# Performance work log

Measured on AMD Instinct MI355X. Metric: run time of the kernel, lower is better.

## Reference

```python
import jax, jax.numpy as jnp
import numpy as np

N, E, G, H, C, DIN, DE = 20000, 320000, 32, 8, 56, 32, 5
HC = H * C  # 448
NEG_SLOPE = 0.2
EPS_BN = 1e-5


def _seg_softmax(scores, seg, num):
    # scores: [E, H], softmax over edges sharing the same target node
    m = jax.ops.segment_max(scores, seg, num_segments=num)
    e = jnp.exp(scores - m[seg])
    s = jax.ops.segment_sum(e, seg, num_segments=num)
    return e / (s[seg] + 1e-16)


def _add_self_loops(src, dst, eattr, n):
    # PyG fill_value='mean': self-loop edge_attr = mean of incoming edge_attr
    deg = jax.ops.segment_sum(jnp.ones((src.shape[0],), eattr.dtype), dst, num_segments=n)
    esum = jax.ops.segment_sum(eattr, dst, num_segments=n)
    loop_attr = esum / jnp.maximum(deg, 1.0)[:, None]
    ar = jnp.arange(n, dtype=src.dtype)
    return (jnp.concatenate([src, ar]), jnp.concatenate([dst, ar]),
            jnp.concatenate([eattr, loop_attr], axis=0))


def _gatv2(x, src, dst, eattr, Wl, Wr, We, att, bias, n):
    xl = (x @ Wl).reshape(n, H, C)  # source transform (messages)
    xr = (x @ Wr).reshape(n, H, C)  # target transform
    ee = (eattr @ We).reshape(-1, H, C)
    s = jax.nn.leaky_relu(xl[src] + xr[dst] + ee, NEG_SLOPE)  # [E, H, C]
    score = jnp.einsum('ehc,hc->eh', s, att)
    alpha = _seg_softmax(score, dst, n)
    out = jax.ops.segment_sum(alpha[..., None] * xl[src], dst, num_segments=n)
    return out.reshape(n, HC) + bias


def _bn(x, gamma, beta):
    m = x.mean(axis=0)
    v = x.var(axis=0)  # biased variance, as torch BatchNorm1d (training)
    return (x - m) * jax.lax.rsqrt(v + EPS_BN) * gamma + beta


def setup_inputs() -> dict:
    key = jax.random.key(0)
    ks = jax.random.split(key, 18)
    sc = lambda k, shape: (jax.random.normal(k, shape, jnp.float32) * 0.05)
    return {
        'x': jax.random.normal(ks[0], (N, DIN), jnp.float32),
        'edge_index': jax.random.randint(ks[1], (2, E), 0, N),
        'edge_attr': jax.random.normal(ks[2], (E, DE), jnp.float32),
        'batch': jnp.sort(jax.random.randint(ks[3], (N,), 0, G)),
        'Wl1': sc(ks[4], (DIN, HC)), 'Wr1': sc(ks[5], (DIN, HC)),
        'We1': sc(ks[6], (DE, HC)), 'att1': sc(ks[7], (H, C)),
        'bias1': jnp.zeros((HC,), jnp.float32),
        'Wl2': sc(ks[8], (HC, HC)), 'Wr2': sc(ks[9], (HC, HC)),
        'We2': sc(ks[10], (DE, HC)), 'att2': sc(ks[11], (H, C)),
        'bias2': jnp.zeros((HC,), jnp.float32),
        'bn_gamma': jnp.ones((HC,), jnp.float32),
        'bn_beta': jnp.zeros((HC,), jnp.float32),
        'Wlin': sc(ks[12], (HC, 18)),
        'blin': jnp.zeros((18,), jnp.float32),
    }


def reference(x, edge_index, edge_attr, batch, Wl1, Wr1, We1, att1, bias1,
              Wl2, Wr2, We2, att2, bias2, bn_gamma, bn_beta, Wlin, blin):
    src, dst = edge_index[0], edge_index[1]
    src2, dst2, ea2 = _add_self_loops(src, dst, edge_attr, N)
    # dropout is identity in eval
    h = _gatv2(x, src2, dst2, ea2, Wl1, Wr1, We1, att1, bias1, N)
    h = jax.nn.elu(h)
    h = _bn(h, bn_gamma, bn_beta)
    h = _gatv2(h, src2, dst2, ea2, Wl2, Wr2, We2, att2, bias2, N)
    # global mean pool per graph
    cnt = jax.ops.segment_sum(jnp.ones((N,), h.dtype), batch, num_segments=G)
    pooled = jax.ops.segment_sum(h, batch, num_segments=G) / jnp.maximum(cnt, 1.0)[:, None]
    pooled = _bn(pooled, bn_gamma, bn_beta)
    logits = pooled @ Wlin + blin
    return jax.nn.log_softmax(logits, axis=1)
```

## Files before the change

kernel.cpp:

```cpp
#include <hip/hip_runtime.h>
#include <hip/hip_bf16.h>

#define NN   20000
#define EE   320000
#define EN   340000
#define HH   8
#define CC   56
#define HC   448
#define DEA  5
#define EAS  8
#define DINN 32
#define GG   32
#define NEG  0.2f

#define PS   512
#define PSS  1024
#define MT   157
#define NT   7
#define SS   896

typedef short bf16x8 __attribute__((ext_vector_type(8)));
typedef float f32x4  __attribute__((ext_vector_type(4)));
typedef float f32x8  __attribute__((ext_vector_type(8)));

static __device__ __forceinline__ unsigned short f2bf(float f) {
  unsigned int u = __float_as_uint(f);
  u += 0x7fffu + ((u >> 16) & 1u);
  return (unsigned short)(u >> 16);
}

static __device__ __forceinline__ f32x8 bf8_to_f32x8(uint4 u) {
  f32x8 o;
  o[0] = __uint_as_float(u.x << 16); o[1] = __uint_as_float(u.x & 0xffff0000u);
  o[2] = __uint_as_float(u.y << 16); o[3] = __uint_as_float(u.y & 0xffff0000u);
  o[4] = __uint_as_float(u.z << 16); o[5] = __uint_as_float(u.z & 0xffff0000u);
  o[6] = __uint_as_float(u.w << 16); o[7] = __uint_as_float(u.w & 0xffff0000u);
  return o;
}

__global__ void k_deg(const int* __restrict__ dst, int* deg) {
  int e = blockIdx.x * 256 + threadIdx.x;
  if (e < EE) atomicAdd(&deg[dst[e]], 1);
}

__global__ __launch_bounds__(1024) void k_scan(const int* __restrict__ deg, int* offs,
                                               int* cursor) {
  __shared__ int tot[1024];
  int t = threadIdx.x;
  int base = t * 20;
  int loc[20];
  int s = 0;
  #pragma unroll
  for (int i = 0; i < 20; i++) {
    int idx = base + i;
    int v = (idx < NN) ? deg[idx] + 1 : 0;
    loc[i] = s;
    s += v;
  }
  tot[t] = s;
  __syncthreads();
  for (int o = 1; o < 1024; o <<= 1) {
    int v = (t >= o) ? tot[t - o] : 0;
    __syncthreads();
    tot[t] += v;
    __syncthreads();
  }
  int basesum = (t == 0) ? 0 : tot[t - 1];
  #pragma unroll
  for (int i = 0; i < 20; i++) {
    int idx = base + i;
    if (idx < NN) { offs[idx] = basesum + loc[i]; cursor[idx] = basesum + loc[i]; }
  }
  if (t == 1023) offs[NN] = tot[1023];
}

__global__ void k_scatter(const int* __restrict__ src, const int* __restrict__ dst,
                          const float* __restrict__ ea,
                          int* cursor, int* __restrict__ csr_src, float* __restrict__ csr_ea) {
  int i = blockIdx.x * 256 + threadIdx.x;
  if (i >= EE) return;
  int d = dst[i], s = src[i];
  float a[DEA];
  #pragma unroll
  for (int j = 0; j < DEA; j++) a[j] = ea[(size_t)i * DEA + j];
  int pos = atomicAdd(&cursor[d], 1);
  csr_src[pos] = s;
  float* o = csr_ea + (size_t)pos * EAS;
  #pragma unroll
  for (int j = 0; j < DEA; j++) o[j] = a[j];
}

#define XCN (NN * DINN)
#define W1N (SS * DINN)
#define W2N (SS * HC)
__global__ void k_aux(const int* __restrict__ offs,
                      int* __restrict__ csr_src, float* __restrict__ csr_ea,
                      const float* __restrict__ x, unsigned short* __restrict__ xb,
                      const float* __restrict__ Wl1, const float* __restrict__ Wr1,
                      unsigned short* __restrict__ W1t,
                      const float* __restrict__ Wl2, const float* __restrict__ Wr2,
                      unsigned short* __restrict__ W2t) {
  int i = blockIdx.x * 256 + threadIdx.x;
  if (i < NN) {
    int n = i;
    int e0 = offs[n], e1 = offs[n + 1] - 1;
    float a0 = 0.f, a1 = 0.f, a2 = 0.f, a3 = 0.f, a4 = 0.f;
    for (int e = e0; e < e1; e++) {
      const float* p = csr_ea + (size_t)e * EAS;
      a0 += p[0]; a1 += p[1]; a2 += p[2]; a3 += p[3]; a4 += p[4];
    }
    float inv = 1.f / fmaxf((float)(e1 - e0), 1.f);
    csr_src[e1] = n;
    float* o = csr_ea + (size_t)e1 * EAS;
    o[0] = a0 * inv; o[1] = a1 * inv; o[2] = a2 * inv; o[3] = a3 * inv; o[4] = a4 * inv;
    return;
  }
  i -= NN;
  if (i < XCN) { xb[i] = f2bf(x[i]); return; }
  i -= XCN;
  if (i < W1N) {
    int k = i / SS, col = i - k * SS;
    int cc = (col < HC) ? col : col - HC;
    const float* W = (col < HC) ? Wl1 : Wr1;
    W1t[(size_t)col * DINN + k] = f2bf(W[(size_t)k * HC + cc]);
    return;
  }
  i -= W1N;
  if (i < W2N) {
    int k = i / SS, col = i - k * SS;
    int cc = (col < HC) ? col : col - HC;
    const float* W = (col < HC) ? Wl2 : Wr2;
    W2t[(size_t)col * HC + k] = f2bf(W[(size_t)k * HC + cc]);
  }
}

__global__ __launch_bounds__(256) void k_gemm1(const unsigned short* __restrict__ xb,
                                               const unsigned short* __restrict__ W1t,
                                               unsigned short* __restrict__ out) {
  int w = threadIdx.x >> 6, lane = threadIdx.x & 63;
  int q = lane >> 4, r = lane & 15;
  int m0 = (blockIdx.x * 4 + w) * 16;
  int n0 = blockIdx.y * 64;
  int arow = m0 + r; if (arow >= NN) arow = NN - 1;
  bf16x8 a = *(const bf16x8*)(xb + (size_t)arow * DINN + q * 8);
  #pragma unroll
  for (int j = 0; j < 4; j++) {
    bf16x8 b = *(const bf16x8*)(W1t + (size_t)(n0 + j * 16 + r) * DINN + q * 8);
    f32x4 acc = {0.f, 0.f, 0.f, 0.f};
    acc = __builtin_amdgcn_mfma_f32_16x16x32_bf16(a, b, acc, 0, 0, 0);
    int col = n0 + j * 16 + r;
    int cp = col + 8 * (col / 56);
    #pragma unroll
    for (int reg = 0; reg < 4; reg++) {
      int row = m0 + q * 4 + reg;
      if (row < NN) out[(size_t)row * PSS + cp] = f2bf(acc[reg]);
    }
  }
}

__global__ __launch_bounds__(256) void k_attn(
    const unsigned short* __restrict__ xlr,
    const int* __restrict__ offs, const int* __restrict__ csr_src,
    const float* __restrict__ csr_ea,
    const float* __restrict__ We, const float* __restrict__ att,
    const float* __restrict__ bias,
    unsigned short* __restrict__ outb, float* __restrict__ outf, int layer1) {
  int n = blockIdx.x * 4 + (threadIdx.x >> 6);
  if (n >= NN) return;
  int lane = threadIdx.x & 63;
  int head = lane >> 3, sub = lane & 7;
  bool v = sub < 7;
  int pc = head * 64 + sub * 8;
  int cr = head * 56 + (v ? sub : 6) * 8;

  f32x8 z = {0.f,0.f,0.f,0.f,0.f,0.f,0.f,0.f};
  f32x8 xr = bf8_to_f32x8(*(const uint4*)(xlr + (size_t)n * PSS + PS + pc));
  f32x8 at = *(const f32x8*)(att + cr);
  if (!v) at = z;
  f32x8 w0 = *(const f32x8*)(We + 0 * HC + cr);
  f32x8 w1 = *(const f32x8*)(We + 1 * HC + cr);
  f32x8 w2 = *(const f32x8*)(We + 2 * HC + cr);
  f32x8 w3 = *(const f32x8*)(We + 3 * HC + cr);
  f32x8 w4 = *(const f32x8*)(We + 4 * HC + cr);

  int e0 = offs[n], e1 = offs[n + 1];
  float l = 0.f;
  f32x8 acc = z;

  for (int e = e0; e < e1; e += 2) {
    int eb = e + 1;
    bool h2v = eb < e1;
    int ebc = h2v ? eb : e;
    int s0 = csr_src[e];
    int s1 = csr_src[ebc];
    const float* ep0 = csr_ea + (size_t)e * EAS;
    const float* ep1 = csr_ea + (size_t)ebc * EAS;
    f32x4 ea0 = *(const f32x4*)ep0;  float e40 = ep0[4];
    f32x4 ea1 = *(const f32x4*)ep1;  float e41 = ep1[4];
    uint4 g0 = *(const uint4*)(xlr + (size_t)s0 * PSS + pc);
    uint4 g1 = *(const uint4*)(xlr + (size_t)s1 * PSS + pc);
    f32x8 xl0 = bf8_to_f32x8(g0);
    f32x8 xl1 = bf8_to_f32x8(g1);

    f32x8 t0 = xl0 + xr;
    t0 += ea0.x * w0; t0 += ea0.y * w1; t0 += ea0.z * w2; t0 += ea0.w * w3; t0 += e40 * w4;
    f32x8 t1 = xl1 + xr;
    t1 += ea1.x * w0; t1 += ea1.y * w1; t1 += ea1.z * w2; t1 += ea1.w * w3; t1 += e41 * w4;
    #pragma unroll
    for (int i = 0; i < 8; i++) {
      t0[i] = fmaxf(t0[i], NEG * t0[i]);
      t1[i] = fmaxf(t1[i], NEG * t1[i]);
    }
    float p0 = 0.f, p1 = 0.f;
    #pragma unroll
    for (int i = 0; i < 8; i++) { p0 += t0[i] * at[i]; p1 += t1[i] * at[i]; }
    p0 += __shfl_xor(p0, 1, 64);  p1 += __shfl_xor(p1, 1, 64);
    p0 += __shfl_xor(p0, 2, 64);  p1 += __shfl_xor(p1, 2, 64);
    p0 += __shfl_xor(p0, 4, 64);  p1 += __shfl_xor(p1, 4, 64);
    float wv0 = __expf(fminf(p0, 60.f));
    float wv1 = h2v ? __expf(fminf(p1, 60.f)) : 0.f;
    acc += wv0 * xl0;
    acc += wv1 * xl1;
    l += wv0 + wv1;
  }

  f32x8 b8 = *(const f32x8*)(bias + cr);
  f32x8 o = acc * (1.f / (l + 1e-16f)) + b8;
  if (layer1) {
    #pragma unroll
    for (int i = 0; i < 8; i++) o[i] = o[i] > 0.f ? o[i] : (__expf(o[i]) - 1.f);
    uint4 pk;
    pk.x = ((unsigned int)f2bf(o[1]) << 16) | f2bf(o[0]);
    pk.y = ((unsigned int)f2bf(o[3]) << 16) | f2bf(o[2]);
    pk.z = ((unsigned int)f2bf(o[5]) << 16) | f2bf(o[4]);
    pk.w = ((unsigned int)f2bf(o[7]) << 16) | f2bf(o[6]);
    if (!v) pk = (uint4){0u, 0u, 0u, 0u};
    *(uint4*)(outb + (size_t)n * PS + pc) = pk;
  } else if (v) {
    float* dst = outf + (size_t)n * HC + cr;
    *(f32x4*)dst       = (f32x4){o[0], o[1], o[2], o[3]};
    *(f32x4*)(dst + 4) = (f32x4){o[4], o[5], o[6], o[7]};
  }
}

__global__ __launch_bounds__(448) void k_bnstats(const unsigned short* __restrict__ h,
                                                 float* stat) {
  int c = threadIdx.x;
  int cp = c + 8 * (c / 56);
  int rows_per = (NN + gridDim.x - 1) / gridDim.x;
  int r0 = blockIdx.x * rows_per, r1 = min(NN, r0 + rows_per);
  float s = 0.f, sq = 0.f;
  for (int r = r0; r < r1; r++) {
    unsigned int u = h[(size_t)r * PS + cp];
    float v = __uint_as_float(u << 16);
    s += v; sq += v * v;
  }
  atomicAdd(&stat[c], s);
  atomicAdd(&stat[HC + c], sq);
}

__global__ __launch_bounds__(64) void k_w2fix(const unsigned short* __restrict__ W2t,
                                              const float* __restrict__ stat,
                                              const float* __restrict__ gam,
                                              const float* __restrict__ bet,
                                              unsigned short* __restrict__ W2s,
                                              float* __restrict__ bias2) {
  int j = blockIdx.x;
  int t = threadIdx.x;
  float bacc = 0.f;
  #pragma unroll
  for (int it = 0; it < 7; it++) {
    int k = t + it * 64;
    float w = __uint_as_float((unsigned int)W2t[(size_t)j * HC + k] << 16);
    float mean = stat[k] * (1.f / NN);
    float var  = stat[HC + k] * (1.f / NN) - mean * mean;
    float sc = rsqrtf(var + 1e-5f) * gam[k];
    float sh = bet[k] - mean * sc;
    bacc += sh * w;
    int kp = k + 8 * (k / 56);
    W2s[(size_t)j * PS + kp] = f2bf(sc * w);
  }
  W2s[(size_t)j * PS + (t >> 3) * 64 + 56 + (t & 7)] = 0;
  #pragma unroll
  for (int m = 32; m >= 1; m >>= 1) bacc += __shfl_xor(bacc, m, 64);
  if (t == 0) bias2[j] = bacc;
}

__global__ __launch_bounds__(256) void k_gemm2(const unsigned short* __restrict__ A,
                                               const unsigned short* __restrict__ Bt,
                                               const float* __restrict__ bias2,
                                               unsigned short* __restrict__ out) {
  __shared__ unsigned short As[128 * 64];
  __shared__ unsigned short Bs[128 * 64];
  int bid = blockIdx.x;
  int g = bid / 56, rem = bid - g * 56;
  int xs = min(8, MT - g * 8);
  int bx = g * 8 + rem % xs;
  int by = rem / xs;
  int t = threadIdx.x;
  int w = t >> 6, lane = t & 63;
  int wm = w >> 1, wn = w & 1;
  int q = lane >> 4, r = lane & 15;
  int m0 = bx * 128;
  int n0 = by * 128;

  const unsigned short *ag[4], *bg[4];
  unsigned short *la[4], *lb[4];
  #pragma unroll
  for (int j = 0; j < 4; j++) {
    int s = t + j * 256;
    int row = s >> 3, part = s & 7;
    int ar = m0 + row; if (ar >= NN) ar = NN - 1;
    ag[j] = A + (size_t)ar * PS + part * 8;
    bg[j] = Bt + (size_t)(n0 + row) * PS + part * 8;
    la[j] = As + s * 8;
    lb[j] = Bs + s * 8;
  }

  f32x4 zero = {0.f, 0.f, 0.f, 0.f};
  f32x4 acc[4][4];
  #pragma unroll
  for (int i = 0; i < 4; i++)
    #pragma unroll
    for (int j = 0; j < 4; j++) acc[i][j] = zero;

  for (int k0 = 0; k0 < PS; k0 += 64) {
    #pragma unroll
    for (int j = 0; j < 4; j++) {
      __builtin_amdgcn_global_load_lds(
          (const __attribute__((address_space(1))) unsigned int*)(ag[j] + k0),
          (__attribute__((address_space(3))) unsigned int*)la[j], 16, 0, 0);
      __builtin_amdgcn_global_load_lds(
          (const __attribute__((address_space(1))) unsigned int*)(bg[j] + k0),
          (__attribute__((address_space(3))) unsigned int*)lb[j], 16, 0, 0);
    }
    __syncthreads();
    #pragma unroll
    for (int kk = 0; kk < 64; kk += 32) {
      bf16x8 af[4], bf[4];
      #pragma unroll
      for (int i = 0; i < 4; i++)
        af[i] = *(const bf16x8*)(As + (wm * 64 + i * 16 + r) * 64 + kk + q * 8);
      #pragma unroll
      for (int j = 0; j < 4; j++)
        bf[j] = *(const bf16x8*)(Bs + (wn * 64 + j * 16 + r) * 64 + kk + q * 8);
      #pragma unroll
      for (int i = 0; i < 4; i++)
        #pragma unroll
        for (int j = 0; j < 4; j++)
          acc[i][j] = __builtin_amdgcn_mfma_f32_16x16x32_bf16(af[i], bf[j], acc[i][j], 0, 0, 0);
    }
    __syncthreads();
  }

  #pragma unroll
  for (int j = 0; j < 4; j++) {
    int col = n0 + wn * 64 + j * 16 + r;
    int cp = col + 8 * (col / 56);
    float bs = bias2[col];
    #pragma unroll
    for (int i = 0; i < 4; i++) {
      int row_base = m0 + wm * 64 + i * 16 + q * 4;
      #pragma unroll
      for (int reg = 0; reg < 4; reg++) {
        int row = row_base + reg;
        if (row < NN) out[(size_t)row * PSS + cp] = f2bf(acc[i][j][reg] + bs);
      }
    }
  }
}

__global__ __launch_bounds__(448) void k_pool(const float* __restrict__ h2,
                                              const int* __restrict__ batch,
                                              float* pooled, int* cnt) {
  int c = threadIdx.x;
  int rows_per = (NN + gridDim.x - 1) / gridDim.x;
  int r0 = blockIdx.x * rows_per, r1 = min(NN, r0 + rows_per);
  if (r0 >= r1) return;
  float loc = 0.f;
  int rc = 0;
  int gcur = batch[r0];
  for (int r = r0; r < r1; r++) {
    int g = batch[r];
    if (g != gcur) {
      atomicAdd(&pooled[gcur * HC + c], loc);
      if (c == 0) atomicAdd(&cnt[gcur], rc);
      loc = 0.f; rc = 0; gcur = g;
    }
    loc += h2[(size_t)r * HC + c];
    rc++;
  }
  atomicAdd(&pooled[gcur * HC + c], loc);
  if (c == 0) atomicAdd(&cnt[gcur], rc);
}

__global__ __launch_bounds__(448) void k_final(const float* __restrict__ pooled_sum,
                                               const int* __restrict__ cnt,
                                               const float* __restrict__ gam,
                                               const float* __restrict__ bet,
                                               const float* __restrict__ Wlin,
                                               const float* __restrict__ blin,
                                               float* __restrict__ out) {
  __shared__ float P[GG * HC];
  __shared__ float L[GG * 18];
  __shared__ float red[GG];
  int c = threadIdx.x;
  float s = 0.f, sq = 0.f;
  for (int g = 0; g < GG; g++) {
    float v = pooled_sum[g * HC + c] / fmaxf((float)cnt[g], 1.f);
    P[g * HC + c] = v; s += v; sq += v * v;
  }
  float mean = s * (1.f / GG);
  float var  = sq * (1.f / GG) - mean * mean;
  float sc = rsqrtf(var + 1e-5f) * gam[c];
  float sh = bet[c] - mean * sc;
  for (int g = 0; g < GG; g++) P[g * HC + c] = P[g * HC + c] * sc + sh;
  __syncthreads();
  for (int o = c; o < GG * 18; o += HC) {
    int g = o / 18, j = o - g * 18;
    float acc = blin[j];
    for (int k = 0; k < HC; k++) acc += P[g * HC + k] * Wlin[k * 18 + j];
    L[o] = acc;
  }
  __syncthreads();
  if (c < GG) {
    float mx = -3.4e38f;
    for (int j = 0; j < 18; j++) mx = fmaxf(mx, L[c * 18 + j]);
    float se = 0.f;
    for (int j = 0; j < 18; j++) se += __expf(L[c * 18 + j] - mx);
    red[c] = mx + logf(se);
  }
  __syncthreads();
  for (int o = c; o < GG * 18; o += HC) out[o] = L[o] - red[o / 18];
}

extern "C" void kernel_launch(void* const* d_in, const int* in_sizes, int n_in,
                              void* d_out, int out_size, void* d_ws, size_t ws_size,
                              hipStream_t stream) {
  (void)in_sizes; (void)n_in; (void)out_size; (void)ws_size;
  const float* x     = (const float*)d_in[0];
  const int*   ei    = (const int*)d_in[1];
  const float* ea    = (const float*)d_in[2];
  const int*   batch = (const int*)d_in[3];
  const float* Wl1   = (const float*)d_in[4];
  const float* Wr1   = (const float*)d_in[5];
  const float* We1   = (const float*)d_in[6];
  const float* att1  = (const float*)d_in[7];
  const float* bias1 = (const float*)d_in[8];
  const float* Wl2   = (const float*)d_in[9];
  const float* Wr2   = (const float*)d_in[10];
  const float* We2   = (const float*)d_in[11];
  const float* att2  = (const float*)d_in[12];
  const float* bias2in = (const float*)d_in[13];
  const float* gam   = (const float*)d_in[14];
  const float* bet   = (const float*)d_in[15];
  const float* Wlin  = (const float*)d_in[16];
  const float* blin  = (const float*)d_in[17];
  float* out = (float*)d_out;
  const int* srcp = ei;
  const int* dstp = ei + EE;

  char* ws = (char*)d_ws;
  size_t off = 0;
  auto alloc = [&](size_t bytes) -> char* {
    char* p = ws + off;
    off = (off + bytes + 255) & ~(size_t)255;
    return p;
  };
  int*   deg     = (int*)  alloc(NN * 4);
  float* bnstat  = (float*)alloc(HC * 2 * 4);
  float* pooled  = (float*)alloc(GG * HC * 4 + GG * 4);
  int*   cnt     = (int*)(pooled + GG * HC);
  size_t zlen    = (size_t)((char*)(cnt + GG) - (char*)deg);

  int*   offs    = (int*)  alloc((NN + 1) * 4);
  int*   cursor  = (int*)  alloc(NN * 4);
  int*   csr_src = (int*)  alloc((size_t)EN * 4);
  float* csr_ea  = (float*)alloc((size_t)EN * EAS * 4);
  unsigned short* xlr = (unsigned short*)alloc((size_t)NN * PSS * 2);
  unsigned short* h1b = (unsigned short*)alloc((size_t)NN * PS * 2);
  float* h1f     = (float*)alloc((size_t)NN * HC * 4);
  unsigned short* xb  = (unsigned short*)alloc((size_t)NN * DINN * 2);
  unsigned short* W1t = (unsigned short*)alloc((size_t)SS * DINN * 2);
  unsigned short* W2t = (unsigned short*)alloc((size_t)SS * HC * 2);
  unsigned short* W2s = (unsigned short*)alloc((size_t)SS * PS * 2);
  float* bias2   = (float*)alloc(SS * 4);

  hipMemsetAsync(deg, 0, zlen, stream);
  k_deg<<<(EE + 255) / 256, 256, 0, stream>>>(dstp, deg);
  k_scan<<<1, 1024, 0, stream>>>(deg, offs, cursor);
  k_scatter<<<(EE + 255) / 256, 256, 0, stream>>>(srcp, dstp, ea, cursor, csr_src, csr_ea);
  k_aux<<<(NN + XCN + W1N + W2N + 255) / 256, 256, 0, stream>>>(
      offs, csr_src, csr_ea, x, xb, Wl1, Wr1, W1t, Wl2, Wr2, W2t);

  dim3 g1((NN + 63) / 64, SS / 64);
  k_gemm1<<<g1, 256, 0, stream>>>(xb, W1t, xlr);
  k_attn<<<(NN + 3) / 4, 256, 0, stream>>>(xlr, offs, csr_src, csr_ea,
                                           We1, att1, bias1, h1b, h1f, 1);
  k_bnstats<<<256, HC, 0, stream>>>(h1b, bnstat);
  k_w2fix<<<SS, 64, 0, stream>>>(W2t, bnstat, gam, bet, W2s, bias2);

  k_gemm2<<<MT * NT, 256, 0, stream>>>(h1b, W2s, bias2, xlr);
  k_attn<<<(NN + 3) / 4, 256, 0, stream>>>(xlr, offs, csr_src, csr_ea,
                                           We2, att2, bias2in, h1b, h1f, 0);

  k_pool<<<640, HC, 0, stream>>>(h1f, batch, pooled, cnt);
  k_final<<<1, HC, 0, stream>>>(pooled, cnt, gam, bet, Wlin, blin, out);
}
```

Before: 473.9 us.

## Drop padded per-head layout and unroll attention edge loop by four

Removes the 64-wide per-head padding (PS/PSS) so xlr, h1b and W2s use dense 448/896 strides. This cuts gather bytes and the GEMM2 K loop from 512 to 448. The attention kernel now processes four edges per iteration with all loads issued first, to expose more memory-level parallelism. The weight transpose in k_aux is also reordered to write coalesced. Unpadded rows make each head's 16-byte gathers no longer 128-byte aligned, which may cost some extra cache-line touches per head.

```diff
diff --git a/kernel.cpp b/kernel.cpp
--- a/kernel.cpp
+++ b/kernel.cpp
@@ -13,11 +13,9 @@
 #define GG   32
 #define NEG  0.2f
 
-#define PS   512
-#define PSS  1024
+#define SS   896
 #define MT   157
 #define NT   7
-#define SS   896
 
 typedef short bf16x8 __attribute__((ext_vector_type(8)));
 typedef float f32x4  __attribute__((ext_vector_type(4)));
@@ -119,18 +117,18 @@
   if (i < XCN) { xb[i] = f2bf(x[i]); return; }
   i -= XCN;
   if (i < W1N) {
-    int k = i / SS, col = i - k * SS;
+    int col = i / DINN, k = i - col * DINN;
     int cc = (col < HC) ? col : col - HC;
     const float* W = (col < HC) ? Wl1 : Wr1;
-    W1t[(size_t)col * DINN + k] = f2bf(W[(size_t)k * HC + cc]);
+    W1t[i] = f2bf(W[(size_t)k * HC + cc]);
     return;
   }
   i -= W1N;
   if (i < W2N) {
-    int k = i / SS, col = i - k * SS;
+    int col = i / HC, k = i - col * HC;
     int cc = (col < HC) ? col : col - HC;
     const float* W = (col < HC) ? Wl2 : Wr2;
-    W2t[(size_t)col * HC + k] = f2bf(W[(size_t)k * HC + cc]);
+    W2t[i] = f2bf(W[(size_t)k * HC + cc]);
   }
 }
 
@@ -149,11 +147,10 @@
     f32x4 acc = {0.f, 0.f, 0.f, 0.f};
     acc = __builtin_amdgcn_mfma_f32_16x16x32_bf16(a, b, acc, 0, 0, 0);
     int col = n0 + j * 16 + r;
-    int cp = col + 8 * (col / 56);
     #pragma unroll
     for (int reg = 0; reg < 4; reg++) {
       int row = m0 + q * 4 + reg;
-      if (row < NN) out[(size_t)row * PSS + cp] = f2bf(acc[reg]);
+      if (row < NN) out[(size_t)row * SS + col] = f2bf(acc[reg]);
     }
   }
 }
@@ -170,74 +167,73 @@
   int lane = threadIdx.x & 63;
   int head = lane >> 3, sub = lane & 7;
   bool v = sub < 7;
-  int pc = head * 64 + sub * 8;
-  int cr = head * 56 + (v ? sub : 6) * 8;
+  int cb = head * 56 + (v ? sub : 6) * 8;
 
   f32x8 z = {0.f,0.f,0.f,0.f,0.f,0.f,0.f,0.f};
-  f32x8 xr = bf8_to_f32x8(*(const uint4*)(xlr + (size_t)n * PSS + PS + pc));
-  f32x8 at = *(const f32x8*)(att + cr);
+  f32x8 xr = bf8_to_f32x8(*(const uint4*)(xlr + (size_t)n * SS + HC + cb));
+  f32x8 at = *(const f32x8*)(att + cb);
   if (!v) at = z;
-  f32x8 w0 = *(const f32x8*)(We + 0 * HC + cr);
-  f32x8 w1 = *(const f32x8*)(We + 1 * HC + cr);
-  f32x8 w2 = *(const f32x8*)(We + 2 * HC + cr);
-  f32x8 w3 = *(const f32x8*)(We + 3 * HC + cr);
-  f32x8 w4 = *(const f32x8*)(We + 4 * HC + cr);
+  f32x8 w0 = *(const f32x8*)(We + 0 * HC + cb);
+  f32x8 w1 = *(const f32x8*)(We + 1 * HC + cb);
+  f32x8 w2 = *(const f32x8*)(We + 2 * HC + cb);
+  f32x8 w3 = *(const f32x8*)(We + 3 * HC + cb);
+  f32x8 w4 = *(const f32x8*)(We + 4 * HC + cb);
 
   int e0 = offs[n], e1 = offs[n + 1];
   float l = 0.f;
   f32x8 acc = z;
 
-  for (int e = e0; e < e1; e += 2) {
-    int eb = e + 1;
-    bool h2v = eb < e1;
-    int ebc = h2v ? eb : e;
-    int s0 = csr_src[e];
-    int s1 = csr_src[ebc];
-    const float* ep0 = csr_ea + (size_t)e * EAS;
-    const float* ep1 = csr_ea + (size_t)ebc * EAS;
-    f32x4 ea0 = *(const f32x4*)ep0;  float e40 = ep0[4];
-    f32x4 ea1 = *(const f32x4*)ep1;  float e41 = ep1[4];
-    uint4 g0 = *(const uint4*)(xlr + (size_t)s0 * PSS + pc);
-    uint4 g1 = *(const uint4*)(xlr + (size_t)s1 * PSS + pc);
-    f32x8 xl0 = bf8_to_f32x8(g0);
-    f32x8 xl1 = bf8_to_f32x8(g1);
-
-    f32x8 t0 = xl0 + xr;
-    t0 += ea0.x * w0; t0 += ea0.y * w1; t0 += ea0.z * w2; t0 += ea0.w * w3; t0 += e40 * w4;
-    f32x8 t1 = xl1 + xr;
-    t1 += ea1.x * w0; t1 += ea1.y * w1; t1 += ea1.z * w2; t1 += ea1.w * w3; t1 += e41 * w4;
-    #pragma unroll
-    for (int i = 0; i < 8; i++) {
-      t0[i] = fmaxf(t0[i], NEG * t0[i]);
-      t1[i] = fmaxf(t1[i], NEG * t1[i]);
-    }
-    float p0 = 0.f, p1 = 0.f;
-    #pragma unroll
-    for (int i = 0; i < 8; i++) { p0 += t0[i] * at[i]; p1 += t1[i] * at[i]; }
-    p0 += __shfl_xor(p0, 1, 64);  p1 += __shfl_xor(p1, 1, 64);
-    p0 += __shfl_xor(p0, 2, 64);  p1 += __shfl_xor(p1, 2, 64);
-    p0 += __shfl_xor(p0, 4, 64);  p1 += __shfl_xor(p1, 4, 64);
-    float wv0 = __expf(fminf(p0, 60.f));
-    float wv1 = h2v ? __expf(fminf(p1, 60.f)) : 0.f;
-    acc += wv0 * xl0;
-    acc += wv1 * xl1;
-    l += wv0 + wv1;
-  }
-
-  f32x8 b8 = *(const f32x8*)(bias + cr);
+  for (int e = e0; e < e1; e += 4) {
+    uint4 g[4];
+    f32x4 eav[4];
+    float ea4[4], wvm[4];
+    #pragma unroll
+    for (int u = 0; u < 4; u++) {
+      int t_ = e + u;
+      bool ok = t_ < e1;
+      int ec = ok ? t_ : e;
+      int s = csr_src[ec];
+      g[u] = *(const uint4*)(xlr + (size_t)s * SS + cb);
+      const float* ep = csr_ea + (size_t)ec * EAS;
+      eav[u] = *(const f32x4*)ep;
+      ea4[u] = ep[4];
+      wvm[u] = ok ? 1.f : 0.f;
+    }
+    #pragma unroll
+    for (int u = 0; u < 4; u++) {
+      f32x8 xl = bf8_to_f32x8(g[u]);
+      f32x8 t = xl + xr;
+      t += eav[u].x * w0; t += eav[u].y * w1; t += eav[u].z * w2;
+      t += eav[u].w * w3; t += ea4[u] * w4;
+      #pragma unroll
+      for (int i = 0; i < 8; i++) t[i] = fmaxf(t[i], NEG * t[i]);
+      float p = 0.f;
+      #pragma unroll
+      for (int i = 0; i < 8; i++) p += t[i] * at[i];
+      p += __shfl_xor(p, 1, 64);
+      p += __shfl_xor(p, 2, 64);
+      p += __shfl_xor(p, 4, 64);
+      float wv = __expf(fminf(p, 60.f)) * wvm[u];
+      acc += wv * xl;
+      l += wv;
+    }
+  }
+
+  f32x8 b8 = *(const f32x8*)(bias + cb);
   f32x8 o = acc * (1.f / (l + 1e-16f)) + b8;
   if (layer1) {
-    #pragma unroll
-    for (int i = 0; i < 8; i++) o[i] = o[i] > 0.f ? o[i] : (__expf(o[i]) - 1.f);
-    uint4 pk;
-    pk.x = ((unsigned int)f2bf(o[1]) << 16) | f2bf(o[0]);
-    pk.y = ((unsigned int)f2bf(o[3]) << 16) | f2bf(o[2]);
-    pk.z = ((unsigned int)f2bf(o[5]) << 16) | f2bf(o[4]);
-    pk.w = ((unsigned int)f2bf(o[7]) << 16) | f2bf(o[6]);
-    if (!v) pk = (uint4){0u, 0u, 0u, 0u};
-    *(uint4*)(outb + (size_t)n * PS + pc) = pk;
+    if (v) {
+      #pragma unroll
+      for (int i = 0; i < 8; i++) o[i] = o[i] > 0.f ? o[i] : (__expf(o[i]) - 1.f);
+      uint4 pk;
+      pk.x = ((unsigned int)f2bf(o[1]) << 16) | f2bf(o[0]);
+      pk.y = ((unsigned int)f2bf(o[3]) << 16) | f2bf(o[2]);
+      pk.z = ((unsigned int)f2bf(o[5]) << 16) | f2bf(o[4]);
+      pk.w = ((unsigned int)f2bf(o[7]) << 16) | f2bf(o[6]);
+      *(uint4*)(outb + (size_t)n * HC + cb) = pk;
+    }
   } else if (v) {
-    float* dst = outf + (size_t)n * HC + cr;
+    float* dst = outf + (size_t)n * HC + cb;
     *(f32x4*)dst       = (f32x4){o[0], o[1], o[2], o[3]};
     *(f32x4*)(dst + 4) = (f32x4){o[4], o[5], o[6], o[7]};
   }
@@ -246,12 +242,11 @@
 __global__ __launch_bounds__(448) void k_bnstats(const unsigned short* __restrict__ h,
                                                  float* stat) {
   int c = threadIdx.x;
-  int cp = c + 8 * (c / 56);
   int rows_per = (NN + gridDim.x - 1) / gridDim.x;
   int r0 = blockIdx.x * rows_per, r1 = min(NN, r0 + rows_per);
   float s = 0.f, sq = 0.f;
   for (int r = r0; r < r1; r++) {
-    unsigned int u = h[(size_t)r * PS + cp];
+    unsigned int u = h[(size_t)r * HC + c];
     float v = __uint_as_float(u << 16);
     s += v; sq += v * v;
   }
@@ -277,10 +272,8 @@
     float sc = rsqrtf(var + 1e-5f) * gam[k];
     float sh = bet[k] - mean * sc;
     bacc += sh * w;
-    int kp = k + 8 * (k / 56);
-    W2s[(size_t)j * PS + kp] = f2bf(sc * w);
-  }
-  W2s[(size_t)j * PS + (t >> 3) * 64 + 56 + (t & 7)] = 0;
+    W2s[(size_t)j * HC + k] = f2bf(sc * w);
+  }
   #pragma unroll
   for (int m = 32; m >= 1; m >>= 1) bacc += __shfl_xor(bacc, m, 64);
   if (t == 0) bias2[j] = bacc;
@@ -311,8 +304,8 @@
     int s = t + j * 256;
     int row = s >> 3, part = s & 7;
     int ar = m0 + row; if (ar >= NN) ar = NN - 1;
-    ag[j] = A + (size_t)ar * PS + part * 8;
-    bg[j] = Bt + (size_t)(n0 + row) * PS + part * 8;
+    ag[j] = A + (size_t)ar * HC + part * 8;
+    bg[j] = Bt + (size_t)(n0 + row) * HC + part * 8;
     la[j] = As + s * 8;
     lb[j] = Bs + s * 8;
   }
@@ -324,7 +317,7 @@
     #pragma unroll
     for (int j = 0; j < 4; j++) acc[i][j] = zero;
 
-  for (int k0 = 0; k0 < PS; k0 += 64) {
+  for (int k0 = 0; k0 < HC; k0 += 64) {
     #pragma unroll
     for (int j = 0; j < 4; j++) {
       __builtin_amdgcn_global_load_lds(
@@ -356,7 +349,6 @@
   #pragma unroll
   for (int j = 0; j < 4; j++) {
     int col = n0 + wn * 64 + j * 16 + r;
-    int cp = col + 8 * (col / 56);
     float bs = bias2[col];
     #pragma unroll
     for (int i = 0; i < 4; i++) {
@@ -364,7 +356,7 @@
       #pragma unroll
       for (int reg = 0; reg < 4; reg++) {
         int row = row_base + reg;
-        if (row < NN) out[(size_t)row * PSS + cp] = f2bf(acc[i][j][reg] + bs);
+        if (row < NN) out[(size_t)row * SS + col] = f2bf(acc[i][j][reg] + bs);
       }
     }
   }
@@ -477,13 +469,13 @@
   int*   cursor  = (int*)  alloc(NN * 4);
   int*   csr_src = (int*)  alloc((size_t)EN * 4);
   float* csr_ea  = (float*)alloc((size_t)EN * EAS * 4);
-  unsigned short* xlr = (unsigned short*)alloc((size_t)NN * PSS * 2);
-  unsigned short* h1b = (unsigned short*)alloc((size_t)NN * PS * 2);
+  unsigned short* xlr = (unsigned short*)alloc((size_t)NN * SS * 2);
+  unsigned short* h1b = (unsigned short*)alloc((size_t)NN * HC * 2);
   float* h1f     = (float*)alloc((size_t)NN * HC * 4);
   unsigned short* xb  = (unsigned short*)alloc((size_t)NN * DINN * 2);
   unsigned short* W1t = (unsigned short*)alloc((size_t)SS * DINN * 2);
   unsigned short* W2t = (unsigned short*)alloc((size_t)SS * HC * 2);
-  unsigned short* W2s = (unsigned short*)alloc((size_t)SS * PS * 2);
+  unsigned short* W2s = (unsigned short*)alloc((size_t)SS * HC * 2);
   float* bias2   = (float*)alloc(SS * 4);
 
   hipMemsetAsync(deg, 0, zlen, stream);
```

New measurement: 505.6 us. +6.7%, slower.
